# Kernel tuning notes

Hardware: AMD Instinct MI355X
Metric: run time of the kernel (lower is better)

The kernel has to match this reference:

```python
import jax, jax.numpy as jnp
import numpy as np
from jax import nn as jnn

N = 100000      # nodes
E = 3200000     # edges (avg degree 32)
G = 1024        # graphs in batch
F_IN = 3        # num_features (hard-coded in module)
D = 32          # dim (hard-coded in module)
BN_EPS = 1e-5


def setup_inputs() -> dict:
    key = jax.random.key(0)
    ks = jax.random.split(key, 24)
    def lin(k, i, o):
        return (jax.random.normal(k, (i, o), jnp.float32) / np.sqrt(i)).astype(jnp.float32)
    inp = {}
    inp["x"] = jax.random.normal(ks[0], (N, F_IN), jnp.float32)
    inp["edge_index"] = jax.random.randint(ks[1], (2, E), 0, N, dtype=jnp.int32)
    inp["batch"] = jnp.sort(jax.random.randint(ks[2], (N,), 0, G, dtype=jnp.int32))
    idx = 3
    in_dims = [F_IN, D, D]
    for l in (1, 2, 3):
        inp[f"W{l}a"] = lin(ks[idx], in_dims[l - 1], D); idx += 1
        inp[f"b{l}a"] = jnp.zeros((D,), jnp.float32)
        inp[f"W{l}b"] = lin(ks[idx], D, D); idx += 1
        inp[f"b{l}b"] = jnp.zeros((D,), jnp.float32)
        inp[f"g{l}"] = jnp.ones((D,), jnp.float32)            # BN gamma
        inp[f"be{l}"] = jnp.zeros((D,), jnp.float32)          # BN beta
        inp[f"m{l}"] = 0.1 * jax.random.normal(ks[idx], (D,), jnp.float32); idx += 1  # running mean
        inp[f"v{l}"] = jax.random.uniform(ks[idx], (D,), jnp.float32, 0.5, 1.5); idx += 1  # running var
    inp["Wf1"] = lin(ks[idx], D, D); idx += 1
    inp["bf1"] = jnp.zeros((D,), jnp.float32)
    inp["Wf2"] = lin(ks[idx], D, 1)
    inp["bf2"] = jnp.zeros((1,), jnp.float32)
    return inp


def reference(x, edge_index, batch,
              W1a, b1a, W1b, b1b, g1, be1, m1, v1,
              W2a, b2a, W2b, b2b, g2, be2, m2, v2,
              W3a, b3a, W3b, b3b, g3, be3, m3, v3,
              Wf1, bf1, Wf2, bf2):
    src, dst = edge_index[0], edge_index[1]

    def gin_bn(h, Wa, ba, Wb, bb, g, be, m, v):
        # GINConv (eps=0): nn(x + sum_{j->i} x_j); then relu; then BatchNorm1d (eval stats)
        agg = jax.ops.segment_sum(h[src], dst, num_segments=N) + h  # [N, d]
        h2 = jnn.relu(agg @ Wa + ba) @ Wb + bb                      # 2-layer MLP
        h2 = jnn.relu(h2)
        return g * (h2 - m) * jax.lax.rsqrt(v + BN_EPS) + be

    h = gin_bn(x, W1a, b1a, W1b, b1b, g1, be1, m1, v1)
    h = gin_bn(h, W2a, b2a, W2b, b2b, g2, be2, m2, v2)
    h = gin_bn(h, W3a, b3a, W3b, b3b, g3, be3, m3, v3)
    p = jax.ops.segment_sum(h, batch, num_segments=G)   # global_add_pool -> [G, D]
    p = jnn.relu(p @ Wf1 + bf1)
    # dropout p=0.5 is identity at inference
    return jnp.tanh(p @ Wf2 + bf2)                      # [G, 1]
```

## Files before the change

kernel.cpp:

```cpp
#include <hip/hip_runtime.h>
#include <math.h>

#define D 32
#define BN_EPS 1e-5f
#define NRANGE 512
#define RWC 196
#define MAXD 80
#define EPB 8192
#define K1_TPB 512
#define EPT (EPB / K1_TPB)

__global__ __launch_bounds__(K1_TPB) void build_part(
    const int* __restrict__ src, const int* __restrict__ dst,
    unsigned int* __restrict__ part, int* __restrict__ gcount,
    int E, int cap, int RW, unsigned long long M) {
    __shared__ unsigned int sorted[EPB];
    __shared__ unsigned short rid[EPB];
    __shared__ int cnt[NRANGE];
    __shared__ int exc[NRANGE];
    __shared__ int cur[NRANGE];
    __shared__ int gbase[NRANGE];
    int t = threadIdx.x;
    cnt[t] = 0;
    __syncthreads();

    int base = blockIdx.x * EPB;
    int n = min(EPB, E - base);

    unsigned int mypk[EPT];
    unsigned short myr[EPT];
#pragma unroll
    for (int k = 0; k < EPT; k++) {
        int i = t + k * K1_TPB;
        if (i < n) {
            int d = dst[base + i];
            int s = src[base + i];
            int r = (int)(((unsigned long long)d * M) >> 40);
            mypk[k] = ((unsigned)(d - r * RW) << 17) | (unsigned)s;
            myr[k] = (unsigned short)r;
            atomicAdd(&cnt[r], 1);
        } else myr[k] = 0xFFFFu;
    }
    __syncthreads();

    int inc = cnt[t];
    exc[t] = inc;
    __syncthreads();
    for (int s = 1; s < NRANGE; s <<= 1) {
        int u = (t >= s) ? exc[t - s] : 0;
        __syncthreads();
        exc[t] += u;
        __syncthreads();
    }
    int excl = exc[t] - cnt[t];
    __syncthreads();
    exc[t] = excl;
    cur[t] = excl;
    gbase[t] = atomicAdd(&gcount[t], cnt[t]);
    __syncthreads();

#pragma unroll
    for (int k = 0; k < EPT; k++) {
        if (myr[k] != 0xFFFFu) {
            int j = atomicAdd(&cur[myr[k]], 1);
            sorted[j] = mypk[k];
            rid[j] = myr[k];
        }
    }
    __syncthreads();

    for (int j = t; j < n; j += K1_TPB) {
        int r = rid[j];
        int pos = gbase[r] + (j - exc[r]);
        if (pos < cap) part[(size_t)r * cap + pos] = sorted[j];
    }
}

__global__ __launch_bounds__(1024) void build_csr(
    const unsigned int* __restrict__ part, const int* __restrict__ gcount,
    int* __restrict__ col, int* __restrict__ deg,
    const float* __restrict__ x, const float* __restrict__ W1a, float* __restrict__ y,
    int cap, int RW, int N, int maxd) {
    __shared__ int bucket[RWC * MAXD];
    __shared__ int rank_[RWC];
    int r = blockIdx.x, t = threadIdx.x, T = blockDim.x;
    for (int i = t; i < RW; i += T) rank_[i] = 0;
    __syncthreads();

    int count = gcount[r]; if (count > cap) count = cap;
    const unsigned int* p = part + (size_t)r * cap;
    int nbase = r * RW;
    for (int i = t; i < count; i += T) {
        unsigned int v = p[i];
        int dl = (int)(v >> 17);
        int slot = atomicAdd(&rank_[dl], 1);
        if (slot < maxd) bucket[dl * maxd + slot] = (int)(v & 0x1FFFFu);
    }
    __syncthreads();

    for (int i = t; i < RW; i += T) {
        int rk = rank_[i]; if (rk > maxd) rk = maxd;
        int pdg = (rk + 7) & ~7; if (pdg > maxd) pdg = maxd;
        int self = nbase + i;
        for (int k = rk; k < pdg; k++) bucket[i * maxd + k] = self;
    }
    __syncthreads();

    int nvalid = N - nbase; if (nvalid > RW) nvalid = RW;
    if (nvalid <= 0) return;
    int words = nvalid * maxd;
    int4* dst4 = (int4*)&col[(size_t)nbase * maxd];
    const int4* src4 = (const int4*)bucket;
    int nq = words >> 2;
    for (int i = t; i < nq; i += T) dst4[i] = src4[i];
    for (int i = t; i < nvalid; i += T) {
        int rk = rank_[i];
        deg[nbase + i] = rk < maxd ? rk : maxd;
    }

    int gidx = t >> 5, lane = t & 31;
    for (int nl = gidx; nl < nvalid; nl += 32) {
        int node = nbase + nl;
        float x0 = x[node * 3 + 0], x1 = x[node * 3 + 1], x2 = x[node * 3 + 2];
        float tv = x0 * W1a[0 * D + lane];
        tv = fmaf(x1, W1a[1 * D + lane], tv);
        tv = fmaf(x2, W1a[2 * D + lane], tv);
        y[(size_t)node * D + lane] = tv;
    }
}

__device__ __forceinline__ float gsum32(const float* __restrict__ hin, int creg, int lane) {
    float a[32];
#pragma unroll
    for (int k = 0; k < 32; k++) {
        int idx = __shfl(creg, k, 32);
        a[k] = hin[idx * D + lane];
    }
#pragma unroll
    for (int st = 1; st < 32; st <<= 1)
#pragma unroll
        for (int k = 0; k < 32; k += (st << 1)) a[k] += a[k + st];
    return a[0];
}

__device__ __forceinline__ float gsum16(const float* __restrict__ hin, int creg, int off,
                                        int lane) {
    float a[16];
#pragma unroll
    for (int k = 0; k < 16; k++) {
        int idx = __shfl(creg, off + k, 32);
        a[k] = hin[idx * D + lane];
    }
#pragma unroll
    for (int st = 1; st < 16; st <<= 1)
#pragma unroll
        for (int k = 0; k < 16; k += (st << 1)) a[k] += a[k + st];
    return a[0];
}

__device__ __forceinline__ float gsum8(const float* __restrict__ hin, int creg, int off,
                                       int lane) {
    float a[8];
#pragma unroll
    for (int k = 0; k < 8; k++) {
        int idx = __shfl(creg, off + k, 32);
        a[k] = hin[idx * D + lane];
    }
#pragma unroll
    for (int st = 1; st < 8; st <<= 1)
#pragma unroll
        for (int k = 0; k < 8; k += (st << 1)) a[k] += a[k + st];
    return a[0];
}

template <bool SKIP_WA, bool POOL>
__global__ __launch_bounds__(256) void layer_fused(
    const float* __restrict__ hin, const int* __restrict__ deg,
    const int* __restrict__ col, int maxd,
    const float* __restrict__ Wa, const float* __restrict__ ba,
    const float* __restrict__ Wb, const float* __restrict__ bb,
    const float* __restrict__ g, const float* __restrict__ be,
    const float* __restrict__ m, const float* __restrict__ v,
    float* __restrict__ hout, const int* __restrict__ batch,
    float* __restrict__ pool, int N) {
    long long gid = (long long)blockIdx.x * blockDim.x + threadIdx.x;
    int i = (int)(gid >> 5);
    int lane = (int)(gid & 31);
    bool valid = i < N;
    if (!POOL && !valid) return;

    float res = 0.f;
    int bg = -1;
    if (valid) {
        int dg = __builtin_nontemporal_load(deg + i);
        if (dg > maxd) dg = maxd;
        int pdg = (dg + 7) & ~7; if (pdg > maxd) pdg = maxd;
        float acc = hin[(size_t)i * D + lane] * (float)(1 + dg - pdg);
        const int* cp = &col[(size_t)i * maxd];

        int cA = __builtin_nontemporal_load(cp + lane);
        int cB = 0, cC = 0;
        if (pdg > 32) cB = __builtin_nontemporal_load(cp + 32 + lane);
        if (pdg > 64) cC = __builtin_nontemporal_load(cp + 64 + (lane & 15));

        float s = 0.f;
        int rem = pdg;
        if (rem >= 32) { s += gsum32(hin, cA, lane); rem -= 32; }
        if (rem >= 32) { s += gsum32(hin, cB, lane); rem -= 32; }
        int cR = (pdg < 32) ? cA : ((pdg < 64) ? cB : cC);
        if (rem & 16) s += gsum16(hin, cR, 0, lane);
        if (rem & 8)  s += gsum8(hin, cR, (rem & 16) ? 16 : 0, lane);
        acc += s;

        float t;
        if (SKIP_WA) {
            t = fmaxf(acc + ba[lane], 0.f);
        } else {
            float t0 = ba[lane], t1 = 0.f, t2 = 0.f, t3 = 0.f;
#pragma unroll
            for (int k = 0; k < D; k += 4) {
                t0 = fmaf(__shfl(acc, k + 0, D), Wa[(k + 0) * D + lane], t0);
                t1 = fmaf(__shfl(acc, k + 1, D), Wa[(k + 1) * D + lane], t1);
                t2 = fmaf(__shfl(acc, k + 2, D), Wa[(k + 2) * D + lane], t2);
                t3 = fmaf(__shfl(acc, k + 3, D), Wa[(k + 3) * D + lane], t3);
            }
            t = fmaxf((t0 + t1) + (t2 + t3), 0.f);
        }
        float o0 = bb[lane], o1 = 0.f, o2 = 0.f, o3 = 0.f;
#pragma unroll
        for (int j = 0; j < D; j += 4) {
            o0 = fmaf(__shfl(t, j + 0, D), Wb[(j + 0) * D + lane], o0);
            o1 = fmaf(__shfl(t, j + 1, D), Wb[(j + 1) * D + lane], o1);
            o2 = fmaf(__shfl(t, j + 2, D), Wb[(j + 2) * D + lane], o2);
            o3 = fmaf(__shfl(t, j + 3, D), Wb[(j + 3) * D + lane], o3);
        }
        float o = fmaxf((o0 + o1) + (o2 + o3), 0.f);
        res = g[lane] * (o - m[lane]) * rsqrtf(v[lane] + BN_EPS) + be[lane];
        if (POOL) bg = __builtin_nontemporal_load(batch + i);
        else __builtin_nontemporal_store(res, &hout[(size_t)i * D + lane]);
    }

    if (POOL) {
        float other = __shfl_xor(res, 32, 64);
        int bo = __shfl_xor(bg, 32, 64);
        bool lowhalf = ((threadIdx.x & 32) == 0);
        if (bg >= 0) {
            if (bg == bo) {
                if (lowhalf) atomicAdd(&pool[(size_t)bg * D + lane], res + other);
            } else {
                atomicAdd(&pool[(size_t)bg * D + lane], res);
            }
        }
    }
}

__global__ void head_kernel(const float* __restrict__ pool, const float* __restrict__ Wf1,
                            const float* __restrict__ bf1, const float* __restrict__ Wf2,
                            const float* __restrict__ bf2, float* __restrict__ out, int G) {
    long long gid = (long long)blockIdx.x * blockDim.x + threadIdx.x;
    int gi = (int)(gid >> 5);
    int lane = (int)(gid & 31);
    if (gi >= G) return;
    float p = pool[(size_t)gi * D + lane];
    float q = bf1[lane];
#pragma unroll
    for (int j = 0; j < D; j++) {
        float pj = __shfl(p, j, D);
        q = fmaf(pj, Wf1[j * D + lane], q);
    }
    q = fmaxf(q, 0.f);
    float r = q * Wf2[lane];
#pragma unroll
    for (int off = 16; off; off >>= 1) r += __shfl_xor(r, off, D);
    if (lane == 0) out[gi] = tanhf(r + bf2[0]);
}

extern "C" void kernel_launch(void* const* d_in, const int* in_sizes, int n_in,
                              void* d_out, int out_size, void* d_ws, size_t ws_size,
                              hipStream_t stream) {
    const float* x = (const float*)d_in[0];
    const int* ei = (const int*)d_in[1];
    const int* batch = (const int*)d_in[2];
    const int E = in_sizes[1] / 2;
    const int N = in_sizes[2];
    const int G = out_size;
    const int* src = ei;
    const int* dst = ei + E;

    const float* P[3][8];
    for (int l = 0; l < 3; l++)
        for (int k = 0; k < 8; k++) P[l][k] = (const float*)d_in[3 + 8 * l + k];
    const float* Wf1 = (const float*)d_in[27];
    const float* bf1 = (const float*)d_in[28];
    const float* Wf2 = (const float*)d_in[29];
    const float* bf2 = (const float*)d_in[30];

    const int RW = (N + NRANGE - 1) / NRANGE;
    const unsigned long long M = ((1ull << 40) + RW - 1) / RW;
    int mean = (E + NRANGE - 1) / NRANGE;
    int cap = mean + mean / 8 + 64;
    cap = (cap + 7) & ~7;

    float* ws = (float*)d_ws;
    size_t off = 0;
    float* h0 = ws + off; off += (size_t)N * D;
    float* h1 = ws + off; off += (size_t)N * D;
    unsigned int* part = (unsigned int*)(ws + off); off += (size_t)NRANGE * cap;
    int* deg = (int*)(ws + off); off += N;
    int* gcount = (int*)(ws + off); off += NRANGE;
    float* pool = ws + off; off += (size_t)G * D;
    int* col = (int*)(ws + off);
    size_t remaining = ws_size / 4 > off ? ws_size / 4 - off : 0;
    int maxd = (int)(remaining / (size_t)N);
    if (maxd > MAXD) maxd = MAXD;
    maxd &= ~15;
    if (maxd < 16) maxd = 16;

    const int B = 256;
    long long tN32 = (long long)N * D;
    int nbp = (E + EPB - 1) / EPB;

    hipMemsetAsync(gcount, 0, (NRANGE + (size_t)G * D) * sizeof(int), stream);
    build_part<<<nbp, K1_TPB, 0, stream>>>(src, dst, part, gcount, E, cap, RW, M);
    build_csr<<<NRANGE, 1024, 0, stream>>>(part, gcount, col, deg, x, P[0][0], h0,
                                           cap, RW, N, maxd);

    layer_fused<true, false><<<(int)((tN32 + B - 1) / B), B, 0, stream>>>(
        h0, deg, col, maxd, P[0][0], P[0][1], P[0][2], P[0][3],
        P[0][4], P[0][5], P[0][6], P[0][7], h1, nullptr, nullptr, N);

    layer_fused<false, false><<<(int)((tN32 + B - 1) / B), B, 0, stream>>>(
        h1, deg, col, maxd, P[1][0], P[1][1], P[1][2], P[1][3],
        P[1][4], P[1][5], P[1][6], P[1][7], h0, nullptr, nullptr, N);

    layer_fused<false, true><<<(int)((tN32 + B - 1) / B), B, 0, stream>>>(
        h0, deg, col, maxd, P[2][0], P[2][1], P[2][2], P[2][3],
        P[2][4], P[2][5], P[2][6], P[2][7], h1, batch, pool, N);

    head_kernel<<<(int)(((long long)G * D + B - 1) / B), B, 0, stream>>>(
        pool, Wf1, bf1, Wf2, bf2, (float*)d_out, G);
}
```

Baseline: 332.7 us.

## Group each node's neighbor list by source-index quartile for gather locality

The CSR build now counts edges per destination node in four buckets keyed by which quarter of the node range the source falls in, then scatters them in a second pass so each neighbor list is ordered by source quartile. The per-node degree is stored as four packed 8-bit counts, and the layer kernels gather each quartile segment with an 8-wide loop that masks tail slots, replacing the old self-index padding. The intent is to make concurrent gathers across waves touch a narrower slice of the feature array for better cache locality. In exchange there is an extra pass over the partition data with atomics, and the gather loop has more branches and shuffles, with four partially filled 8-groups per node instead of one padded tail.

```diff
diff --git a/kernel.cpp b/kernel.cpp
--- a/kernel.cpp
+++ b/kernel.cpp
@@ -78,45 +78,61 @@
 
 __global__ __launch_bounds__(1024) void build_csr(
     const unsigned int* __restrict__ part, const int* __restrict__ gcount,
-    int* __restrict__ col, int* __restrict__ deg,
+    int* __restrict__ col, unsigned int* __restrict__ tdeg,
     const float* __restrict__ x, const float* __restrict__ W1a, float* __restrict__ y,
-    int cap, int RW, int N, int maxd) {
+    int cap, int RW, int N, int maxd, int q1, int q2, int q3) {
     __shared__ int bucket[RWC * MAXD];
-    __shared__ int rank_[RWC];
+    __shared__ int cnt4[RWC][4];
+    __shared__ int run4[RWC][4];
     int r = blockIdx.x, t = threadIdx.x, T = blockDim.x;
-    for (int i = t; i < RW; i += T) rank_[i] = 0;
+    for (int i = t; i < RW * 4; i += T) ((int*)cnt4)[i] = 0;
     __syncthreads();
 
     int count = gcount[r]; if (count > cap) count = cap;
     const unsigned int* p = part + (size_t)r * cap;
     int nbase = r * RW;
+    int nvalid = N - nbase; if (nvalid > RW) nvalid = RW;
+
     for (int i = t; i < count; i += T) {
         unsigned int v = p[i];
         int dl = (int)(v >> 17);
-        int slot = atomicAdd(&rank_[dl], 1);
-        if (slot < maxd) bucket[dl * maxd + slot] = (int)(v & 0x1FFFFu);
-    }
-    __syncthreads();
-
-    for (int i = t; i < RW; i += T) {
-        int rk = rank_[i]; if (rk > maxd) rk = maxd;
-        int pdg = (rk + 7) & ~7; if (pdg > maxd) pdg = maxd;
-        int self = nbase + i;
-        for (int k = rk; k < pdg; k++) bucket[i * maxd + k] = self;
-    }
-    __syncthreads();
-
-    int nvalid = N - nbase; if (nvalid > RW) nvalid = RW;
+        int sidx = (int)(v & 0x1FFFFu);
+        int tl = (sidx >= q1) + (sidx >= q2) + (sidx >= q3);
+        atomicAdd(&cnt4[dl][tl], 1);
+    }
+    __syncthreads();
+
+    if (t < RW) {
+        int s0 = 0; unsigned int packed = 0;
+#pragma unroll
+        for (int tl = 0; tl < 4; tl++) {
+            int c = cnt4[t][tl];
+            int a = maxd - s0; if (a > c) a = c; if (a < 0) a = 0;
+            run4[t][tl] = s0;
+            cnt4[t][tl] = s0 + a;
+            packed |= (unsigned)a << (8 * tl);
+            s0 += a;
+        }
+        if (t < nvalid) tdeg[nbase + t] = packed;
+    }
+    __syncthreads();
+
+    for (int i = t; i < count; i += T) {
+        unsigned int v = p[i];
+        int dl = (int)(v >> 17);
+        int sidx = (int)(v & 0x1FFFFu);
+        int tl = (sidx >= q1) + (sidx >= q2) + (sidx >= q3);
+        int slot = atomicAdd(&run4[dl][tl], 1);
+        if (slot < cnt4[dl][tl]) bucket[dl * maxd + slot] = sidx;
+    }
+    __syncthreads();
+
     if (nvalid <= 0) return;
     int words = nvalid * maxd;
     int4* dst4 = (int4*)&col[(size_t)nbase * maxd];
     const int4* src4 = (const int4*)bucket;
     int nq = words >> 2;
     for (int i = t; i < nq; i += T) dst4[i] = src4[i];
-    for (int i = t; i < nvalid; i += T) {
-        int rk = rank_[i];
-        deg[nbase + i] = rk < maxd ? rk : maxd;
-    }
 
     int gidx = t >> 5, lane = t & 31;
     for (int nl = gidx; nl < nvalid; nl += 32) {
@@ -129,53 +145,32 @@
     }
 }
 
-__device__ __forceinline__ float gsum32(const float* __restrict__ hin, int creg, int lane) {
-    float a[32];
-#pragma unroll
-    for (int k = 0; k < 32; k++) {
-        int idx = __shfl(creg, k, 32);
-        a[k] = hin[idx * D + lane];
-    }
-#pragma unroll
-    for (int st = 1; st < 32; st <<= 1)
-#pragma unroll
-        for (int k = 0; k < 32; k += (st << 1)) a[k] += a[k + st];
-    return a[0];
-}
-
-__device__ __forceinline__ float gsum16(const float* __restrict__ hin, int creg, int off,
-                                        int lane) {
-    float a[16];
-#pragma unroll
-    for (int k = 0; k < 16; k++) {
-        int idx = __shfl(creg, off + k, 32);
-        a[k] = hin[idx * D + lane];
-    }
-#pragma unroll
-    for (int st = 1; st < 16; st <<= 1)
-#pragma unroll
-        for (int k = 0; k < 16; k += (st << 1)) a[k] += a[k + st];
-    return a[0];
-}
-
-__device__ __forceinline__ float gsum8(const float* __restrict__ hin, int creg, int off,
-                                       int lane) {
-    float a[8];
-#pragma unroll
-    for (int k = 0; k < 8; k++) {
-        int idx = __shfl(creg, off + k, 32);
-        a[k] = hin[idx * D + lane];
-    }
-#pragma unroll
-    for (int st = 1; st < 8; st <<= 1)
-#pragma unroll
-        for (int k = 0; k < 8; k += (st << 1)) a[k] += a[k + st];
-    return a[0];
+__device__ __forceinline__ float tile_gsum(const float* __restrict__ hin,
+                                           int cA, int cB, int cC,
+                                           int start, int end, int lane) {
+    float s = 0.f;
+    for (int base = start; base < end; base += 8) {
+        float a[8];
+#pragma unroll
+        for (int k = 0; k < 8; k++) {
+            int slot = base + k;
+            float val = 0.f;
+            if (slot < end) {
+                int cr = slot < 32 ? cA : (slot < 64 ? cB : cC);
+                int ln = slot < 64 ? (slot & 31) : (slot - 64);
+                int idx = __shfl(cr, ln, 32);
+                val = hin[(size_t)idx * D + lane];
+            }
+            a[k] = val;
+        }
+        s += (((a[0] + a[1]) + (a[2] + a[3])) + ((a[4] + a[5]) + (a[6] + a[7])));
+    }
+    return s;
 }
 
 template <bool SKIP_WA, bool POOL>
 __global__ __launch_bounds__(256) void layer_fused(
-    const float* __restrict__ hin, const int* __restrict__ deg,
+    const float* __restrict__ hin, const unsigned int* __restrict__ tdeg,
     const int* __restrict__ col, int maxd,
     const float* __restrict__ Wa, const float* __restrict__ ba,
     const float* __restrict__ Wb, const float* __restrict__ bb,
@@ -192,25 +187,22 @@
     float res = 0.f;
     int bg = -1;
     if (valid) {
-        int dg = __builtin_nontemporal_load(deg + i);
-        if (dg > maxd) dg = maxd;
-        int pdg = (dg + 7) & ~7; if (pdg > maxd) pdg = maxd;
-        float acc = hin[(size_t)i * D + lane] * (float)(1 + dg - pdg);
+        unsigned int td = __builtin_nontemporal_load(tdeg + i);
+        int c0 = td & 255, c1 = (td >> 8) & 255, c2 = (td >> 16) & 255, c3 = (td >> 24) & 255;
+        int e0 = c0, e1 = e0 + c1, e2 = e1 + c2, e3 = e2 + c3;
+
+        float acc = hin[(size_t)i * D + lane];
         const int* cp = &col[(size_t)i * maxd];
 
         int cA = __builtin_nontemporal_load(cp + lane);
         int cB = 0, cC = 0;
-        if (pdg > 32) cB = __builtin_nontemporal_load(cp + 32 + lane);
-        if (pdg > 64) cC = __builtin_nontemporal_load(cp + 64 + (lane & 15));
-
-        float s = 0.f;
-        int rem = pdg;
-        if (rem >= 32) { s += gsum32(hin, cA, lane); rem -= 32; }
-        if (rem >= 32) { s += gsum32(hin, cB, lane); rem -= 32; }
-        int cR = (pdg < 32) ? cA : ((pdg < 64) ? cB : cC);
-        if (rem & 16) s += gsum16(hin, cR, 0, lane);
-        if (rem & 8)  s += gsum8(hin, cR, (rem & 16) ? 16 : 0, lane);
-        acc += s;
+        if (e3 > 32) cB = __builtin_nontemporal_load(cp + 32 + lane);
+        if (e3 > 64) cC = __builtin_nontemporal_load(cp + 64 + (lane & 15));
+
+        acc += tile_gsum(hin, cA, cB, cC, 0,  e0, lane);
+        acc += tile_gsum(hin, cA, cB, cC, e0, e1, lane);
+        acc += tile_gsum(hin, cA, cB, cC, e1, e2, lane);
+        acc += tile_gsum(hin, cA, cB, cC, e2, e3, lane);
 
         float t;
         if (SKIP_WA) {
@@ -301,12 +293,14 @@
     int cap = mean + mean / 8 + 64;
     cap = (cap + 7) & ~7;
 
+    const int q1 = N / 4, q2 = N / 2, q3 = (3 * N) / 4;
+
     float* ws = (float*)d_ws;
     size_t off = 0;
     float* h0 = ws + off; off += (size_t)N * D;
     float* h1 = ws + off; off += (size_t)N * D;
     unsigned int* part = (unsigned int*)(ws + off); off += (size_t)NRANGE * cap;
-    int* deg = (int*)(ws + off); off += N;
+    unsigned int* tdeg = (unsigned int*)(ws + off); off += N;
     int* gcount = (int*)(ws + off); off += NRANGE;
     float* pool = ws + off; off += (size_t)G * D;
     int* col = (int*)(ws + off);
@@ -322,19 +316,19 @@
 
     hipMemsetAsync(gcount, 0, (NRANGE + (size_t)G * D) * sizeof(int), stream);
     build_part<<<nbp, K1_TPB, 0, stream>>>(src, dst, part, gcount, E, cap, RW, M);
-    build_csr<<<NRANGE, 1024, 0, stream>>>(part, gcount, col, deg, x, P[0][0], h0,
-                                           cap, RW, N, maxd);
+    build_csr<<<NRANGE, 1024, 0, stream>>>(part, gcount, col, tdeg, x, P[0][0], h0,
+                                           cap, RW, N, maxd, q1, q2, q3);
 
     layer_fused<true, false><<<(int)((tN32 + B - 1) / B), B, 0, stream>>>(
-        h0, deg, col, maxd, P[0][0], P[0][1], P[0][2], P[0][3],
+        h0, tdeg, col, maxd, P[0][0], P[0][1], P[0][2], P[0][3],
         P[0][4], P[0][5], P[0][6], P[0][7], h1, nullptr, nullptr, N);
 
     layer_fused<false, false><<<(int)((tN32 + B - 1) / B), B, 0, stream>>>(
-        h1, deg, col, maxd, P[1][0], P[1][1], P[1][2], P[1][3],
+        h1, tdeg, col, maxd, P[1][0], P[1][1], P[1][2], P[1][3],
         P[1][4], P[1][5], P[1][6], P[1][7], h0, nullptr, nullptr, N);
 
     layer_fused<false, true><<<(int)((tN32 + B - 1) / B), B, 0, stream>>>(
-        h0, deg, col, maxd, P[2][0], P[2][1], P[2][2], P[2][3],
+        h0, tdeg, col, maxd, P[2][0], P[2][1], P[2][2], P[2][3],
         P[2][4], P[2][5], P[2][6], P[2][7], h1, batch, pool, N);
 
     head_kernel<<<(int)(((long long)G * D + B - 1) / B), B, 0, stream>>>(
```

Result: slower. 365.3 us (+9.8%).

## Store node features in fp16 and gather half2 pairs split across half-warps

Applied to the files above, without the earlier changes.

Intermediate node feature buffers change from fp32 to fp16, halving the bytes moved by the random neighbour gathers in each GIN layer. The gather is restructured so each lane loads a half2 (two features) and the two half-warps take alternating neighbours, then combine with a shuffle. The dense MLPs are rewritten to match, with each lane handling two output columns and the two halves splitting the input dimension. This trades feature precision for bandwidth, which may fail strict tolerance checks, and some nontemporal loads become ordinary loads.

```diff
diff --git a/kernel.cpp b/kernel.cpp
--- a/kernel.cpp
+++ b/kernel.cpp
@@ -1,4 +1,5 @@
 #include <hip/hip_runtime.h>
+#include <hip/hip_fp16.h>
 #include <math.h>
 
 #define D 32
@@ -79,7 +80,7 @@
 __global__ __launch_bounds__(1024) void build_csr(
     const unsigned int* __restrict__ part, const int* __restrict__ gcount,
     int* __restrict__ col, int* __restrict__ deg,
-    const float* __restrict__ x, const float* __restrict__ W1a, float* __restrict__ y,
+    const float* __restrict__ x, const float* __restrict__ W1a, __half* __restrict__ y,
     int cap, int RW, int N, int maxd) {
     __shared__ int bucket[RWC * MAXD];
     __shared__ int rank_[RWC];
@@ -125,130 +126,146 @@
         float tv = x0 * W1a[0 * D + lane];
         tv = fmaf(x1, W1a[1 * D + lane], tv);
         tv = fmaf(x2, W1a[2 * D + lane], tv);
-        y[(size_t)node * D + lane] = tv;
-    }
-}
-
-__device__ __forceinline__ float gsum32(const float* __restrict__ hin, int creg, int lane) {
-    float a[32];
-#pragma unroll
-    for (int k = 0; k < 32; k++) {
-        int idx = __shfl(creg, k, 32);
-        a[k] = hin[idx * D + lane];
-    }
-#pragma unroll
-    for (int st = 1; st < 32; st <<= 1)
-#pragma unroll
-        for (int k = 0; k < 32; k += (st << 1)) a[k] += a[k + st];
-    return a[0];
-}
-
-__device__ __forceinline__ float gsum16(const float* __restrict__ hin, int creg, int off,
-                                        int lane) {
-    float a[16];
-#pragma unroll
-    for (int k = 0; k < 16; k++) {
-        int idx = __shfl(creg, off + k, 32);
-        a[k] = hin[idx * D + lane];
-    }
-#pragma unroll
-    for (int st = 1; st < 16; st <<= 1)
-#pragma unroll
-        for (int k = 0; k < 16; k += (st << 1)) a[k] += a[k + st];
-    return a[0];
-}
-
-__device__ __forceinline__ float gsum8(const float* __restrict__ hin, int creg, int off,
-                                       int lane) {
-    float a[8];
-#pragma unroll
-    for (int k = 0; k < 8; k++) {
-        int idx = __shfl(creg, off + k, 32);
-        a[k] = hin[idx * D + lane];
-    }
-#pragma unroll
-    for (int st = 1; st < 8; st <<= 1)
-#pragma unroll
-        for (int k = 0; k < 8; k += (st << 1)) a[k] += a[k + st];
-    return a[0];
+        y[(size_t)node * D + lane] = __float2half_rn(tv);
+    }
+}
+
+template <int NP>
+__device__ __forceinline__ void gpairs(const __half* __restrict__ hin, int creg, int poff,
+                                       int half, int p, float& ax, float& ay) {
+    float s0x = 0.f, s0y = 0.f, s1x = 0.f, s1y = 0.f;
+#pragma unroll
+    for (int j = 0; j < NP; j += 2) {
+        int i0 = __shfl(creg, 2 * (poff + j) + half, 32);
+        int i1 = __shfl(creg, 2 * (poff + j + 1) + half, 32);
+        float2 f0 = __half22float2(*(const __half2*)(hin + ((size_t)i0 << 5) + 2 * p));
+        float2 f1 = __half22float2(*(const __half2*)(hin + ((size_t)i1 << 5) + 2 * p));
+        s0x += f0.x; s0y += f0.y;
+        s1x += f1.x; s1y += f1.y;
+    }
+    ax += s0x + s1x;
+    ay += s0y + s1y;
+}
+
+__device__ __forceinline__ void mm_part(const float* __restrict__ W, float inx, float iny,
+                                        int half, int p, float& tx, float& ty) {
+#pragma unroll
+    for (int kk = 0; kk < 8; kk++) {
+        int pair = 8 * half + kk;
+        float a0 = __shfl(inx, pair, 32);
+        float a1 = __shfl(iny, pair, 32);
+        const float* w0 = W + (size_t)(2 * pair) * D + 2 * p;
+        float2 W0 = *(const float2*)w0;
+        float2 W1 = *(const float2*)(w0 + D);
+        tx = fmaf(a0, W0.x, tx); tx = fmaf(a1, W1.x, tx);
+        ty = fmaf(a0, W0.y, ty); ty = fmaf(a1, W1.y, ty);
+    }
 }
 
 template <bool SKIP_WA, bool POOL>
 __global__ __launch_bounds__(256) void layer_fused(
-    const float* __restrict__ hin, const int* __restrict__ deg,
+    const __half* __restrict__ hin, const int* __restrict__ deg,
     const int* __restrict__ col, int maxd,
     const float* __restrict__ Wa, const float* __restrict__ ba,
     const float* __restrict__ Wb, const float* __restrict__ bb,
     const float* __restrict__ g, const float* __restrict__ be,
     const float* __restrict__ m, const float* __restrict__ v,
-    float* __restrict__ hout, const int* __restrict__ batch,
+    __half* __restrict__ hout, const int* __restrict__ batch,
     float* __restrict__ pool, int N) {
     long long gid = (long long)blockIdx.x * blockDim.x + threadIdx.x;
     int i = (int)(gid >> 5);
-    int lane = (int)(gid & 31);
+    int L = (int)(gid & 31);
+    int p = L & 15;
+    int half = L >> 4;
     bool valid = i < N;
     if (!POOL && !valid) return;
 
-    float res = 0.f;
+    float rx = 0.f, ry = 0.f;
     int bg = -1;
     if (valid) {
-        int dg = __builtin_nontemporal_load(deg + i);
+        int dg = deg[i];
         if (dg > maxd) dg = maxd;
         int pdg = (dg + 7) & ~7; if (pdg > maxd) pdg = maxd;
-        float acc = hin[(size_t)i * D + lane] * (float)(1 + dg - pdg);
+
+        float2 selfv = __half22float2(*(const __half2*)(hin + ((size_t)i << 5) + 2 * p));
+        float w = (float)(1 + dg - pdg);
+        float ax = (half == 0) ? w * selfv.x : 0.f;
+        float ay = (half == 0) ? w * selfv.y : 0.f;
+
         const int* cp = &col[(size_t)i * maxd];
-
-        int cA = __builtin_nontemporal_load(cp + lane);
+        int cA = cp[L];
         int cB = 0, cC = 0;
-        if (pdg > 32) cB = __builtin_nontemporal_load(cp + 32 + lane);
-        if (pdg > 64) cC = __builtin_nontemporal_load(cp + 64 + (lane & 15));
-
-        float s = 0.f;
-        int rem = pdg;
-        if (rem >= 32) { s += gsum32(hin, cA, lane); rem -= 32; }
-        if (rem >= 32) { s += gsum32(hin, cB, lane); rem -= 32; }
-        int cR = (pdg < 32) ? cA : ((pdg < 64) ? cB : cC);
-        if (rem & 16) s += gsum16(hin, cR, 0, lane);
-        if (rem & 8)  s += gsum8(hin, cR, (rem & 16) ? 16 : 0, lane);
-        acc += s;
-
-        float t;
+        if (pdg > 32) cB = cp[32 + L];
+        if (pdg > 64) cC = cp[64 + p];
+
+        if (pdg >= 32) gpairs<16>(hin, cA, 0, half, p, ax, ay);
+        if (pdg >= 64) gpairs<16>(hin, cB, 0, half, p, ax, ay);
+        if (pdg & 16) {
+            int st = pdg & ~31;
+            int cr = st < 32 ? cA : (st < 64 ? cB : cC);
+            gpairs<8>(hin, cr, 0, half, p, ax, ay);
+        }
+        if (pdg & 8) {
+            int st = pdg & ~15;
+            int cr = st < 32 ? cA : (st < 64 ? cB : cC);
+            gpairs<4>(hin, cr, (st & 31) >> 1, half, p, ax, ay);
+        }
+        ax += __shfl_xor(ax, 16, 32);
+        ay += __shfl_xor(ay, 16, 32);
+
+        float tx, ty;
         if (SKIP_WA) {
-            t = fmaxf(acc + ba[lane], 0.f);
+            float2 ba2 = *(const float2*)(ba + 2 * p);
+            tx = fmaxf(ax + ba2.x, 0.f);
+            ty = fmaxf(ay + ba2.y, 0.f);
         } else {
-            float t0 = ba[lane], t1 = 0.f, t2 = 0.f, t3 = 0.f;
-#pragma unroll
-            for (int k = 0; k < D; k += 4) {
-                t0 = fmaf(__shfl(acc, k + 0, D), Wa[(k + 0) * D + lane], t0);
-                t1 = fmaf(__shfl(acc, k + 1, D), Wa[(k + 1) * D + lane], t1);
-                t2 = fmaf(__shfl(acc, k + 2, D), Wa[(k + 2) * D + lane], t2);
-                t3 = fmaf(__shfl(acc, k + 3, D), Wa[(k + 3) * D + lane], t3);
-            }
-            t = fmaxf((t0 + t1) + (t2 + t3), 0.f);
-        }
-        float o0 = bb[lane], o1 = 0.f, o2 = 0.f, o3 = 0.f;
-#pragma unroll
-        for (int j = 0; j < D; j += 4) {
-            o0 = fmaf(__shfl(t, j + 0, D), Wb[(j + 0) * D + lane], o0);
-            o1 = fmaf(__shfl(t, j + 1, D), Wb[(j + 1) * D + lane], o1);
-            o2 = fmaf(__shfl(t, j + 2, D), Wb[(j + 2) * D + lane], o2);
-            o3 = fmaf(__shfl(t, j + 3, D), Wb[(j + 3) * D + lane], o3);
-        }
-        float o = fmaxf((o0 + o1) + (o2 + o3), 0.f);
-        res = g[lane] * (o - m[lane]) * rsqrtf(v[lane] + BN_EPS) + be[lane];
-        if (POOL) bg = __builtin_nontemporal_load(batch + i);
-        else __builtin_nontemporal_store(res, &hout[(size_t)i * D + lane]);
+            float px = 0.f, py = 0.f;
+            mm_part(Wa, ax, ay, half, p, px, py);
+            px += __shfl_xor(px, 16, 32);
+            py += __shfl_xor(py, 16, 32);
+            float2 ba2 = *(const float2*)(ba + 2 * p);
+            tx = fmaxf(px + ba2.x, 0.f);
+            ty = fmaxf(py + ba2.y, 0.f);
+        }
+        float ox = 0.f, oy = 0.f;
+        mm_part(Wb, tx, ty, half, p, ox, oy);
+        ox += __shfl_xor(ox, 16, 32);
+        oy += __shfl_xor(oy, 16, 32);
+        float2 bb2 = *(const float2*)(bb + 2 * p);
+        ox = fmaxf(ox + bb2.x, 0.f);
+        oy = fmaxf(oy + bb2.y, 0.f);
+
+        float2 g2 = *(const float2*)(g + 2 * p);
+        float2 be2 = *(const float2*)(be + 2 * p);
+        float2 m2 = *(const float2*)(m + 2 * p);
+        float2 v2 = *(const float2*)(v + 2 * p);
+        rx = g2.x * (ox - m2.x) * rsqrtf(v2.x + BN_EPS) + be2.x;
+        ry = g2.y * (oy - m2.y) * rsqrtf(v2.y + BN_EPS) + be2.y;
+
+        if (POOL) {
+            bg = batch[i];
+        } else if (half == 0) {
+            __half2 hv = __float22half2_rn(make_float2(rx, ry));
+            unsigned int u;
+            __builtin_memcpy(&u, &hv, 4);
+            __builtin_nontemporal_store(u, (unsigned int*)(hout + ((size_t)i << 5) + 2 * p));
+        }
     }
 
     if (POOL) {
-        float other = __shfl_xor(res, 32, 64);
+        float qx = __shfl_xor(rx, 32, 64);
+        float qy = __shfl_xor(ry, 32, 64);
         int bo = __shfl_xor(bg, 32, 64);
-        bool lowhalf = ((threadIdx.x & 32) == 0);
-        if (bg >= 0) {
+        bool low = ((threadIdx.x & 32) == 0);
+        if (bg >= 0 && half == 0) {
             if (bg == bo) {
-                if (lowhalf) atomicAdd(&pool[(size_t)bg * D + lane], res + other);
+                if (low) {
+                    atomicAdd(&pool[(size_t)bg * D + 2 * p + 0], rx + qx);
+                    atomicAdd(&pool[(size_t)bg * D + 2 * p + 1], ry + qy);
+                }
             } else {
-                atomicAdd(&pool[(size_t)bg * D + lane], res);
+                atomicAdd(&pool[(size_t)bg * D + 2 * p + 0], rx);
+                atomicAdd(&pool[(size_t)bg * D + 2 * p + 1], ry);
             }
         }
     }
@@ -303,8 +320,8 @@
 
     float* ws = (float*)d_ws;
     size_t off = 0;
-    float* h0 = ws + off; off += (size_t)N * D;
-    float* h1 = ws + off; off += (size_t)N * D;
+    __half* h0 = (__half*)(ws + off); off += (size_t)N * D / 2;
+    __half* h1 = (__half*)(ws + off); off += (size_t)N * D / 2;
     unsigned int* part = (unsigned int*)(ws + off); off += (size_t)NRANGE * cap;
     int* deg = (int*)(ws + off); off += N;
     int* gcount = (int*)(ws + off); off += NRANGE;
```

New measurement: 356.5 us. 1.07x slower.

## Store node features in fp16 and gather with 16-byte vector loads

Applied to the files above, without the earlier changes.

Intermediate node features h0/h1 are stored as half precision instead of fp32, halving the bytes moved by the neighbor gather, which dominates the layer kernels. The gather is restructured so each lane loads 8 halves (uint4) for one of 8 neighbors at a time, accumulates in fp32, then reduces across lanes with xor shuffles and redistributes for the MLP. This trades some numerical precision (fp16 rounding of activations) for less memory traffic and fewer load instructions.

```diff
diff --git a/kernel.cpp b/kernel.cpp
--- a/kernel.cpp
+++ b/kernel.cpp
@@ -1,4 +1,5 @@
 #include <hip/hip_runtime.h>
+#include <hip/hip_fp16.h>
 #include <math.h>
 
 #define D 32
@@ -9,6 +10,13 @@
 #define EPB 8192
 #define K1_TPB 512
 #define EPT (EPB / K1_TPB)
+
+__device__ __forceinline__ void st_half_nt(__half* p, float v) {
+    __half hv = __float2half_rn(v);
+    unsigned short us;
+    __builtin_memcpy(&us, &hv, 2);
+    __builtin_nontemporal_store(us, (unsigned short*)p);
+}
 
 __global__ __launch_bounds__(K1_TPB) void build_part(
     const int* __restrict__ src, const int* __restrict__ dst,
@@ -79,7 +87,7 @@
 __global__ __launch_bounds__(1024) void build_csr(
     const unsigned int* __restrict__ part, const int* __restrict__ gcount,
     int* __restrict__ col, int* __restrict__ deg,
-    const float* __restrict__ x, const float* __restrict__ W1a, float* __restrict__ y,
+    const float* __restrict__ x, const float* __restrict__ W1a, __half* __restrict__ y,
     int cap, int RW, int N, int maxd) {
     __shared__ int bucket[RWC * MAXD];
     __shared__ int rank_[RWC];
@@ -125,119 +133,118 @@
         float tv = x0 * W1a[0 * D + lane];
         tv = fmaf(x1, W1a[1 * D + lane], tv);
         tv = fmaf(x2, W1a[2 * D + lane], tv);
-        y[(size_t)node * D + lane] = tv;
-    }
-}
-
-__device__ __forceinline__ float gsum32(const float* __restrict__ hin, int creg, int lane) {
-    float a[32];
-#pragma unroll
-    for (int k = 0; k < 32; k++) {
-        int idx = __shfl(creg, k, 32);
-        a[k] = hin[idx * D + lane];
-    }
-#pragma unroll
-    for (int st = 1; st < 32; st <<= 1)
-#pragma unroll
-        for (int k = 0; k < 32; k += (st << 1)) a[k] += a[k + st];
-    return a[0];
-}
-
-__device__ __forceinline__ float gsum16(const float* __restrict__ hin, int creg, int off,
-                                        int lane) {
-    float a[16];
-#pragma unroll
-    for (int k = 0; k < 16; k++) {
-        int idx = __shfl(creg, off + k, 32);
-        a[k] = hin[idx * D + lane];
-    }
-#pragma unroll
-    for (int st = 1; st < 16; st <<= 1)
-#pragma unroll
-        for (int k = 0; k < 16; k += (st << 1)) a[k] += a[k + st];
-    return a[0];
-}
-
-__device__ __forceinline__ float gsum8(const float* __restrict__ hin, int creg, int off,
-                                       int lane) {
-    float a[8];
-#pragma unroll
-    for (int k = 0; k < 8; k++) {
-        int idx = __shfl(creg, off + k, 32);
-        a[k] = hin[idx * D + lane];
-    }
-#pragma unroll
-    for (int st = 1; st < 8; st <<= 1)
-#pragma unroll
-        for (int k = 0; k < 8; k += (st << 1)) a[k] += a[k + st];
-    return a[0];
+        y[(size_t)node * D + lane] = __float2half_rn(tv);
+    }
+}
+
+__device__ __forceinline__ void cvt_add(const uint4& u, float* acc, float wgt) {
+    __half2 h0, h1, h2, h3;
+    __builtin_memcpy(&h0, &u.x, 4);
+    __builtin_memcpy(&h1, &u.y, 4);
+    __builtin_memcpy(&h2, &u.z, 4);
+    __builtin_memcpy(&h3, &u.w, 4);
+    float2 f0 = __half22float2(h0), f1 = __half22float2(h1);
+    float2 f2 = __half22float2(h2), f3 = __half22float2(h3);
+    acc[0] = fmaf(wgt, f0.x, acc[0]); acc[1] = fmaf(wgt, f0.y, acc[1]);
+    acc[2] = fmaf(wgt, f1.x, acc[2]); acc[3] = fmaf(wgt, f1.y, acc[3]);
+    acc[4] = fmaf(wgt, f2.x, acc[4]); acc[5] = fmaf(wgt, f2.y, acc[5]);
+    acc[6] = fmaf(wgt, f3.x, acc[6]); acc[7] = fmaf(wgt, f3.y, acc[7]);
 }
 
 template <bool SKIP_WA, bool POOL>
 __global__ __launch_bounds__(256) void layer_fused(
-    const float* __restrict__ hin, const int* __restrict__ deg,
+    const __half* __restrict__ hin, const int* __restrict__ deg,
     const int* __restrict__ col, int maxd,
     const float* __restrict__ Wa, const float* __restrict__ ba,
     const float* __restrict__ Wb, const float* __restrict__ bb,
     const float* __restrict__ g, const float* __restrict__ be,
     const float* __restrict__ m, const float* __restrict__ v,
-    float* __restrict__ hout, const int* __restrict__ batch,
+    __half* __restrict__ hout, const int* __restrict__ batch,
     float* __restrict__ pool, int N) {
     long long gid = (long long)blockIdx.x * blockDim.x + threadIdx.x;
     int i = (int)(gid >> 5);
-    int lane = (int)(gid & 31);
+    int L = (int)(gid & 31);
+    int k8 = L >> 2;
+    int q = L & 3;
     bool valid = i < N;
     if (!POOL && !valid) return;
 
     float res = 0.f;
     int bg = -1;
     if (valid) {
-        int dg = __builtin_nontemporal_load(deg + i);
+        int dg = deg[i];
         if (dg > maxd) dg = maxd;
         int pdg = (dg + 7) & ~7; if (pdg > maxd) pdg = maxd;
-        float acc = hin[(size_t)i * D + lane] * (float)(1 + dg - pdg);
         const int* cp = &col[(size_t)i * maxd];
 
-        int cA = __builtin_nontemporal_load(cp + lane);
+        int cA = cp[L];
         int cB = 0, cC = 0;
-        if (pdg > 32) cB = __builtin_nontemporal_load(cp + 32 + lane);
-        if (pdg > 64) cC = __builtin_nontemporal_load(cp + 64 + (lane & 15));
-
-        float s = 0.f;
-        int rem = pdg;
-        if (rem >= 32) { s += gsum32(hin, cA, lane); rem -= 32; }
-        if (rem >= 32) { s += gsum32(hin, cB, lane); rem -= 32; }
-        int cR = (pdg < 32) ? cA : ((pdg < 64) ? cB : cC);
-        if (rem & 16) s += gsum16(hin, cR, 0, lane);
-        if (rem & 8)  s += gsum8(hin, cR, (rem & 16) ? 16 : 0, lane);
-        acc += s;
+        if (pdg > 32) cB = cp[32 + L];
+        if (pdg > 64) cC = cp[64 + (L & 15)];
+
+        float acc[8] = {0.f, 0.f, 0.f, 0.f, 0.f, 0.f, 0.f, 0.f};
+        int nb = pdg >> 3;
+        int b = 0;
+        for (; b + 2 <= nb; b += 2) {
+            int s0 = (b << 3) + k8;
+            int s1 = s0 + 8;
+            int cX0 = (s0 < 32) ? cA : ((s0 < 64) ? cB : cC);
+            int cX1 = (s1 < 32) ? cA : ((s1 < 64) ? cB : cC);
+            int i0 = __shfl(cX0, s0 & 31, 32);
+            int i1 = __shfl(cX1, s1 & 31, 32);
+            uint4 u0 = *(const uint4*)(hin + ((size_t)i0 << 5) + (q << 3));
+            uint4 u1 = *(const uint4*)(hin + ((size_t)i1 << 5) + (q << 3));
+            cvt_add(u0, acc, 1.f);
+            cvt_add(u1, acc, 1.f);
+        }
+        if (b < nb) {
+            int s0 = (b << 3) + k8;
+            int cX0 = (s0 < 32) ? cA : ((s0 < 64) ? cB : cC);
+            int i0 = __shfl(cX0, s0 & 31, 32);
+            uint4 u0 = *(const uint4*)(hin + ((size_t)i0 << 5) + (q << 3));
+            cvt_add(u0, acc, 1.f);
+        }
+#pragma unroll
+        for (int r = 0; r < 8; r++) acc[r] += __shfl_xor(acc[r], 4, 32);
+#pragma unroll
+        for (int r = 0; r < 8; r++) acc[r] += __shfl_xor(acc[r], 8, 32);
+#pragma unroll
+        for (int r = 0; r < 8; r++) acc[r] += __shfl_xor(acc[r], 16, 32);
+
+        {
+            uint4 su = *(const uint4*)(hin + ((size_t)i << 5) + (q << 3));
+            cvt_add(su, acc, (float)(1 + dg - pdg));
+        }
 
         float t;
         if (SKIP_WA) {
-            t = fmaxf(acc + ba[lane], 0.f);
+            int qd = L >> 3;
+            float a = __shfl(acc[0], qd, 32);
+#pragma unroll
+            for (int r = 1; r < 8; r++) {
+                float xr = __shfl(acc[r], qd, 32);
+                a = ((L & 7) == r) ? xr : a;
+            }
+            t = fmaxf(a + ba[L], 0.f);
         } else {
-            float t0 = ba[lane], t1 = 0.f, t2 = 0.f, t3 = 0.f;
-#pragma unroll
-            for (int k = 0; k < D; k += 4) {
-                t0 = fmaf(__shfl(acc, k + 0, D), Wa[(k + 0) * D + lane], t0);
-                t1 = fmaf(__shfl(acc, k + 1, D), Wa[(k + 1) * D + lane], t1);
-                t2 = fmaf(__shfl(acc, k + 2, D), Wa[(k + 2) * D + lane], t2);
-                t3 = fmaf(__shfl(acc, k + 3, D), Wa[(k + 3) * D + lane], t3);
+            t = ba[L];
+#pragma unroll
+            for (int d = 0; d < D; d++) {
+                float ad = __shfl(acc[d & 7], d >> 3, 32);
+                t = fmaf(ad, Wa[d * D + L], t);
             }
-            t = fmaxf((t0 + t1) + (t2 + t3), 0.f);
-        }
-        float o0 = bb[lane], o1 = 0.f, o2 = 0.f, o3 = 0.f;
-#pragma unroll
-        for (int j = 0; j < D; j += 4) {
-            o0 = fmaf(__shfl(t, j + 0, D), Wb[(j + 0) * D + lane], o0);
-            o1 = fmaf(__shfl(t, j + 1, D), Wb[(j + 1) * D + lane], o1);
-            o2 = fmaf(__shfl(t, j + 2, D), Wb[(j + 2) * D + lane], o2);
-            o3 = fmaf(__shfl(t, j + 3, D), Wb[(j + 3) * D + lane], o3);
-        }
-        float o = fmaxf((o0 + o1) + (o2 + o3), 0.f);
-        res = g[lane] * (o - m[lane]) * rsqrtf(v[lane] + BN_EPS) + be[lane];
-        if (POOL) bg = __builtin_nontemporal_load(batch + i);
-        else __builtin_nontemporal_store(res, &hout[(size_t)i * D + lane]);
+            t = fmaxf(t, 0.f);
+        }
+        float o = bb[L];
+#pragma unroll
+        for (int j = 0; j < D; j++) {
+            float tj = __shfl(t, j, 32);
+            o = fmaf(tj, Wb[j * D + L], o);
+        }
+        o = fmaxf(o, 0.f);
+        res = g[L] * (o - m[L]) * rsqrtf(v[L] + BN_EPS) + be[L];
+        if (POOL) bg = batch[i];
+        else st_half_nt(&hout[(size_t)i * D + L], res);
     }
 
     if (POOL) {
@@ -246,9 +253,9 @@
         bool lowhalf = ((threadIdx.x & 32) == 0);
         if (bg >= 0) {
             if (bg == bo) {
-                if (lowhalf) atomicAdd(&pool[(size_t)bg * D + lane], res + other);
+                if (lowhalf) atomicAdd(&pool[(size_t)bg * D + L], res + other);
             } else {
-                atomicAdd(&pool[(size_t)bg * D + lane], res);
+                atomicAdd(&pool[(size_t)bg * D + L], res);
             }
         }
     }
@@ -303,8 +310,8 @@
 
     float* ws = (float*)d_ws;
     size_t off = 0;
-    float* h0 = ws + off; off += (size_t)N * D;
-    float* h1 = ws + off; off += (size_t)N * D;
+    __half* h0 = (__half*)(ws + off); off += (size_t)N * D / 2;
+    __half* h1 = (__half*)(ws + off); off += (size_t)N * D / 2;
     unsigned int* part = (unsigned int*)(ws + off); off += (size_t)NRANGE * cap;
     int* deg = (int*)(ws + off); off += N;
     int* gcount = (int*)(ws + off); off += NRANGE;
```

After: 313.9 us. 5.7% less time.
